# Optimization experiments

Hardware: AMD Instinct MI355X
Metric: run time of the kernel (lower is better)

The kernel has to match this reference:

```python
import jax, jax.numpy as jnp
import numpy as np

HIDDEN = 450
DEPTH = 6
ATOM_FDIM = 35          # len(ELEM_LIST)+6+5+1
BOND_FDIM = 5
MAX_NB = 15
N_ATOMS = 20000
N_BONDS = 40000
N_MESS = 16000          # tree messages (row 0 is the zero padding slot)
N_MOLS = 1000


def _linear_init(key, out_dim, in_dim):
    s = 1.0 / np.sqrt(in_dim)
    return jax.random.uniform(key, (out_dim, in_dim), jnp.float32, -s, s)


def setup_inputs() -> dict:
    key = jax.random.key(0)
    ks = jax.random.split(key, 9)
    total_msg = N_MESS + N_BONDS
    fatoms = jax.random.normal(ks[0], (N_ATOMS, ATOM_FDIM), jnp.float32)
    fbonds = jax.random.normal(ks[1], (N_BONDS, ATOM_FDIM + BOND_FDIM), jnp.float32)
    agraph = jax.random.randint(ks[2], (N_ATOMS, MAX_NB), 0, total_msg, jnp.int32)
    bgraph = jax.random.randint(ks[3], (N_BONDS, MAX_NB), 0, total_msg, jnp.int32)
    tree_message = jax.random.normal(ks[4], (N_MESS, HIDDEN), jnp.float32)
    tree_message = tree_message.at[0].set(0.0)  # index 0 = padding message
    # uniform scope: N_MOLS molecules of N_ATOMS//N_MOLS atoms each
    mol_ids = jnp.repeat(jnp.arange(N_MOLS, dtype=jnp.int32), N_ATOMS // N_MOLS)
    W_i = _linear_init(ks[5], HIDDEN, ATOM_FDIM + BOND_FDIM)
    W_h = _linear_init(ks[6], HIDDEN, HIDDEN)
    W_o = _linear_init(ks[7], HIDDEN, ATOM_FDIM + HIDDEN)
    s = 1.0 / np.sqrt(ATOM_FDIM + HIDDEN)
    b_o = jax.random.uniform(ks[8], (HIDDEN,), jnp.float32, -s, s)
    return {"fatoms": fatoms, "fbonds": fbonds, "agraph": agraph, "bgraph": bgraph,
            "mol_ids": mol_ids, "n_mols": N_MOLS, "tree_message": tree_message,
            "W_i": W_i, "W_h": W_h, "W_o": W_o, "b_o": b_o}


def reference(fatoms, fbonds, agraph, bgraph, mol_ids, n_mols, tree_message,
              W_i, W_h, W_o, b_o):
    binput = fbonds @ W_i.T                       # [B, H]
    graph_message = jax.nn.relu(binput)
    for _ in range(DEPTH - 1):                    # static depth loop
        message = jnp.concatenate([tree_message, graph_message], axis=0)  # [M+B, H]
        nei_message = message[bgraph].sum(axis=1)  # gather [B, MAX_NB, H] -> [B, H]
        graph_message = jax.nn.relu(binput + nei_message @ W_h.T)
    message = jnp.concatenate([tree_message, graph_message], axis=0)
    nei_message = message[agraph].sum(axis=1)      # [A, H]
    ainput = jnp.concatenate([fatoms, nei_message], axis=1)  # [A, ATOM_FDIM+H]
    atom_hiddens = jax.nn.relu(ainput @ W_o.T + b_o)          # [A, H]
    # mean over each molecule's atoms (scope)
    sums = jax.ops.segment_sum(atom_hiddens, mol_ids, num_segments=n_mols)
    counts = jax.ops.segment_sum(jnp.ones((atom_hiddens.shape[0], 1), atom_hiddens.dtype),
                                 mol_ids, num_segments=n_mols)
    return sums / counts
```

## Files before the change

### kernel.cpp

```cpp
#include <hip/hip_runtime.h>

#define HIDDEN 450
#define MAX_NB 15
#define N_ATOMS 20000
#define N_BONDS 40000
#define N_MESS  16000
#define N_MOLS  1000
#define KPAD    512
#define MSTRIDE 456

typedef unsigned int uint;
typedef unsigned short ushort;
typedef __bf16 bf16x8 __attribute__((ext_vector_type(8)));
typedef float  f32x4  __attribute__((ext_vector_type(4)));

__device__ __forceinline__ ushort f2bf(float f) {
    uint u = __builtin_bit_cast(uint, f);
    u += 0x7fffu + ((u >> 16) & 1u);
    return (ushort)(u >> 16);
}
__device__ __forceinline__ float bfhi(uint w) {
    return __builtin_bit_cast(float, w & 0xffff0000u);
}
__device__ __forceinline__ float bflo(uint w) {
    return __builtin_bit_cast(float, w << 16);
}


__global__ __launch_bounds__(256) void pack_tree(const float* __restrict__ tree,
                                                 ushort* __restrict__ tbuf) {
    const int r = blockIdx.x, t = threadIdx.x;
    if (t < 228) {
        uint p = 0;
        if (t < 225) {
            const float2 v = *(const float2*)&tree[(size_t)r * HIDDEN + 2 * t];
            p = (uint)f2bf(v.x) | ((uint)f2bf(v.y) << 16);
        }
        ((uint*)(tbuf + (size_t)r * MSTRIDE))[t] = p;
    }
}

__global__ __launch_bounds__(256) void pack_bonds(const float* __restrict__ fbonds,
                                                  ushort* __restrict__ Abuf) {
    const int r = blockIdx.x * 4 + (threadIdx.x >> 6);
    const int t = threadIdx.x & 63;
    if (r >= N_BONDS) return;
    ushort* row = Abuf + (size_t)r * KPAD;
    if (t < 40) row[t] = f2bf(fbonds[(size_t)r * 40 + t]);
    else        row[t] = 0;
    if (t < 16) row[496 + t] = 0;
}

__global__ __launch_bounds__(256) void pack_atoms(const float* __restrict__ fatoms,
                                                  ushort* __restrict__ Aout) {
    const int r = blockIdx.x * 4 + (threadIdx.x >> 6);
    const int t = threadIdx.x & 63;
    if (r >= N_ATOMS) return;
    ushort* row = Aout + (size_t)r * KPAD;
    if (t < 40) row[t] = (t < 35) ? f2bf(fatoms[(size_t)r * 35 + t]) : (ushort)0;
    if (t < 16) row[496 + t] = 0;
}

__global__ __launch_bounds__(256) void pack_w(const float* __restrict__ W_i,
                                              const float* __restrict__ W_h,
                                              const float* __restrict__ W_o,
                                              ushort* __restrict__ Wcat,
                                              ushort* __restrict__ Wocat) {
    const int n = blockIdx.x;
    for (int c = threadIdx.x; c < KPAD; c += 256) {
        float v = 0.0f, vo = 0.0f;
        if (n < HIDDEN) {
            if (c < 40)       v = W_i[(size_t)n * 40 + c];
            else if (c < 490) v = W_h[(size_t)n * HIDDEN + (c - 40)];
            if (c < 35)       vo = W_o[(size_t)n * 485 + c];
            else if (c >= 40 && c < 490) vo = W_o[(size_t)n * 485 + 35 + (c - 40)];
        }
        Wcat [(size_t)n * KPAD + c] = f2bf(v);
        Wocat[(size_t)n * KPAD + c] = f2bf(vo);
    }
}

__global__ __launch_bounds__(256) void precompute_base(const int* __restrict__ g,
                                                       const ushort* __restrict__ tbuf,
                                                       ushort* __restrict__ base,
                                                       int nrows) {
    const int r = blockIdx.x * 4 + (threadIdx.x >> 6);
    const int lane = threadIdx.x & 63;
    if (r >= nrows) return;
    const int* gr = g + (size_t)r * MAX_NB;
    int idx[MAX_NB];
#pragma unroll
    for (int j = 0; j < MAX_NB; ++j) idx[j] = gr[j];
    if (lane >= 57) return;
    const int off = lane * 8;
    float acc[8] = {};
#pragma unroll
    for (int j = 0; j < MAX_NB; ++j) {
        if (idx[j] < N_MESS) {
            const uint4 w = *(const uint4*)(tbuf + (size_t)idx[j] * MSTRIDE + off);
            acc[0] += bflo(w.x); acc[1] += bfhi(w.x);
            acc[2] += bflo(w.y); acc[3] += bfhi(w.y);
            acc[4] += bflo(w.z); acc[5] += bfhi(w.z);
            acc[6] += bflo(w.w); acc[7] += bfhi(w.w);
        }
    }
    uint4 p;
    p.x = (uint)f2bf(acc[0]) | ((uint)f2bf(acc[1]) << 16);
    p.y = (uint)f2bf(acc[2]) | ((uint)f2bf(acc[3]) << 16);
    p.z = (uint)f2bf(acc[4]) | ((uint)f2bf(acc[5]) << 16);
    p.w = (uint)f2bf(acc[6]) | ((uint)f2bf(acc[7]) << 16);
    *(uint4*)(base + (size_t)r * MSTRIDE + off) = p;
}

__global__ __launch_bounds__(256) void gather_dyn(const int* __restrict__ g,
                                                  const ushort* __restrict__ base,
                                                  const ushort* __restrict__ gmsg,
                                                  ushort* __restrict__ dst, int nrows) {
    const int r = blockIdx.x * 4 + (threadIdx.x >> 6);
    const int lane = threadIdx.x & 63;
    if (r >= nrows) return;
    const int* gr = g + (size_t)r * MAX_NB;
    int idx[MAX_NB];
#pragma unroll
    for (int j = 0; j < MAX_NB; ++j) idx[j] = gr[j];
    if (lane >= 57) return;
    const int off = lane * 8;
    const uint4 b = *(const uint4*)(base + (size_t)r * MSTRIDE + off);
    float acc[8];
    acc[0] = bflo(b.x); acc[1] = bfhi(b.x);
    acc[2] = bflo(b.y); acc[3] = bfhi(b.y);
    acc[4] = bflo(b.z); acc[5] = bfhi(b.z);
    acc[6] = bflo(b.w); acc[7] = bfhi(b.w);
#pragma unroll
    for (int j = 0; j < MAX_NB; ++j) {
        if (idx[j] >= N_MESS) {
            const uint4 w = *(const uint4*)(gmsg + (size_t)(idx[j] - N_MESS) * MSTRIDE + off);
            acc[0] += bflo(w.x); acc[1] += bfhi(w.x);
            acc[2] += bflo(w.y); acc[3] += bfhi(w.y);
            acc[4] += bflo(w.z); acc[5] += bfhi(w.z);
            acc[6] += bflo(w.w); acc[7] += bfhi(w.w);
        }
    }
    uint4 p;
    p.x = (uint)f2bf(acc[0]) | ((uint)f2bf(acc[1]) << 16);
    p.y = (uint)f2bf(acc[2]) | ((uint)f2bf(acc[3]) << 16);
    p.z = (uint)f2bf(acc[4]) | ((uint)f2bf(acc[5]) << 16);
    p.w = (uint)f2bf(acc[6]) | ((uint)f2bf(acc[7]) << 16);
    *(uint4*)(dst + (size_t)r * KPAD + 40 + off) = p;
}

template <int MODE, int KT>
__global__ __launch_bounds__(256, 2) void mfma_gemm(
    const ushort* __restrict__ A, int M,
    const ushort* __restrict__ W,
    const float* __restrict__ bias, const int* __restrict__ mol_ids,
    ushort* __restrict__ gout, float* __restrict__ aout, int mtiles) {
    __shared__ ushort At[64 * KT * 32];
    const int tid = threadIdx.x;
    const int id  = blockIdx.x;
    const int b     = id & 7;
    const int n_blk = (id >> 3) & 1;
    const int m_blk = (id >> 4) * 8 + b;
    if (m_blk >= mtiles) return;
    const int m0 = m_blk * 64, n0 = n_blk * 256;
    const int CPR = KT * 4;

    {
        const int srow = tid >> 2;
        const int c0   = tid & 3;
        const ushort* gsrc = A + (size_t)min(m0 + srow, M - 1) * KPAD;
        ushort* lrow = At + srow * (KT * 32);
#pragma unroll
        for (int c = c0; c < CPR; c += 4) {
            const uint4 v = *(const uint4*)(gsrc + c * 8);
            *(uint4*)&lrow[(c ^ (srow & 7)) * 8] = v;
        }
    }
    __syncthreads();

    const int lane = tid & 63;
    const int wave = tid >> 6;
    const int wn = wave * 64;
    const int lr = lane & 15;
    const int lk = lane >> 4;

    size_t woff[4];
#pragma unroll
    for (int s = 0; s < 4; ++s)
        woff[s] = (size_t)(n0 + wn + s * 16 + lr) * KPAD + lk * 8;

    f32x4 acc[4][4];
#pragma unroll
    for (int i = 0; i < 4; ++i)
#pragma unroll
        for (int j = 0; j < 4; ++j) acc[i][j] = (f32x4){0.f, 0.f, 0.f, 0.f};

    bf16x8 wa[4], wb[4], afa[4];
#pragma unroll
    for (int s = 0; s < 4; ++s) wa[s] = *(const bf16x8*)&W[woff[s]];
#pragma unroll
    for (int s = 0; s < 4; ++s)
        wb[s] = (KT > 1) ? *(const bf16x8*)&W[woff[s] + 32] : wa[s];
#pragma unroll
    for (int mt = 0; mt < 4; ++mt) {
        const int row = mt * 16 + lr;
        afa[mt] = *(const bf16x8*)&At[(row * CPR + (lk ^ (row & 7))) * 8];
    }

#pragma unroll
    for (int i = 0; i < KT; ++i) {
        bf16x8 wc[4], afb[4];
        if (i + 2 < KT) {
#pragma unroll
            for (int s = 0; s < 4; ++s)
                wc[s] = *(const bf16x8*)&W[woff[s] + (size_t)(i + 2) * 32];
        }
        if (i + 1 < KT) {
#pragma unroll
            for (int mt = 0; mt < 4; ++mt) {
                const int row = mt * 16 + lr;
                const int chunk = (((i + 1) * 4 + lk)) ^ (row & 7);
                afb[mt] = *(const bf16x8*)&At[(row * CPR + chunk) * 8];
            }
        }
#pragma unroll
        for (int mt = 0; mt < 4; ++mt)
#pragma unroll
            for (int nt = 0; nt < 4; ++nt)
                acc[mt][nt] = __builtin_amdgcn_mfma_f32_16x16x32_bf16(
                    afa[mt], wa[nt], acc[mt][nt], 0, 0, 0);
        if (i + 1 < KT) {
#pragma unroll
            for (int s = 0; s < 4; ++s) wa[s] = wb[s];
#pragma unroll
            for (int mt = 0; mt < 4; ++mt) afa[mt] = afb[mt];
        }
        if (i + 2 < KT) {
#pragma unroll
            for (int s = 0; s < 4; ++s) wb[s] = wc[s];
        }
    }

    const int col_l = lane & 15;
    const int rbase = (lane >> 4) * 4;
#pragma unroll
    for (int mt = 0; mt < 4; ++mt) {
        const int mbase = m0 + mt * 16 + rbase;
        int mol[4];
        if (MODE == 1) {
#pragma unroll
            for (int reg = 0; reg < 4; ++reg)
                mol[reg] = mol_ids[min(mbase + reg, M - 1)];
        }
#pragma unroll
        for (int nt = 0; nt < 4; ++nt) {
            const int n = n0 + wn + nt * 16 + col_l;
            if (MODE == 0) {
#pragma unroll
                for (int reg = 0; reg < 4; ++reg) {
                    const int m = mbase + reg;
                    if (m >= M) continue;
                    if (n < HIDDEN)
                        gout[(size_t)m * MSTRIDE + n] = f2bf(fmaxf(acc[mt][nt][reg], 0.0f));
                    else if (n < MSTRIDE)
                        gout[(size_t)m * MSTRIDE + n] = 0;
                }
            } else {
                if (n >= HIDDEN) continue;
                const float bsum = bias[n];
                float run = 0.0f;
                int cur = mol[0];
#pragma unroll
                for (int reg = 0; reg < 4; ++reg) {
                    const float v = (mbase + reg < M)
                        ? fmaxf(acc[mt][nt][reg] + bsum, 0.0f) : 0.0f;
                    if (mol[reg] != cur) {
                        atomicAdd(&aout[(size_t)cur * HIDDEN + n], run);
                        cur = mol[reg];
                        run = 0.0f;
                    }
                    run += v;
                }
                atomicAdd(&aout[(size_t)cur * HIDDEN + n], run);
            }
        }
    }
}

__global__ __launch_bounds__(256) void count_atoms(const int* __restrict__ mol_ids,
                                                   float* __restrict__ counts) {
    const int a = blockIdx.x * 256 + threadIdx.x;
    if (a < N_ATOMS) atomicAdd(&counts[mol_ids[a]], 1.0f);
}
__global__ __launch_bounds__(256) void div_counts(float* __restrict__ out,
                                                  const float* __restrict__ counts) {
    const int i = blockIdx.x * 256 + threadIdx.x;
    if (i < N_MOLS * HIDDEN) out[i] = out[i] / counts[i / HIDDEN];
}

extern "C" void kernel_launch(void* const* d_in, const int* in_sizes, int n_in,
                              void* d_out, int out_size, void* d_ws, size_t ws_size,
                              hipStream_t stream) {
    const float* fatoms  = (const float*)d_in[0];
    const float* fbonds  = (const float*)d_in[1];
    const int*   agraph  = (const int*)d_in[2];
    const int*   bgraph  = (const int*)d_in[3];
    const int*   mol_ids = (const int*)d_in[4];
    const float* tree    = (const float*)d_in[6];
    const float* W_i     = (const float*)d_in[7];
    const float* W_h     = (const float*)d_in[8];
    const float* W_o     = (const float*)d_in[9];
    const float* b_o     = (const float*)d_in[10];
    float* out = (float*)d_out;

    ushort* Abuf   = (ushort*)d_ws;
    ushort* Aout   = Abuf   + (size_t)N_BONDS * KPAD;
    ushort* gmsg   = Aout   + (size_t)N_ATOMS * KPAD;
    ushort* tbuf   = gmsg   + (size_t)N_BONDS * MSTRIDE;
    ushort* Wcat   = tbuf   + (size_t)N_MESS  * MSTRIDE;
    ushort* Wocat  = Wcat   + (size_t)KPAD * KPAD;
    ushort* base_b = Wocat  + (size_t)KPAD * KPAD;
    ushort* base_a = base_b + (size_t)N_BONDS * MSTRIDE;
    float*  counts = (float*)(base_a + (size_t)N_ATOMS * MSTRIDE);

    (void)hipMemsetAsync(d_out, 0, (size_t)N_MOLS * HIDDEN * sizeof(float), stream);
    (void)hipMemsetAsync(counts, 0, N_MOLS * sizeof(float), stream);

    const dim3 blk(256);
    pack_tree <<<N_MESS, blk, 0, stream>>>(tree, tbuf);
    pack_bonds<<<(N_BONDS + 3) / 4, blk, 0, stream>>>(fbonds, Abuf);
    pack_atoms<<<(N_ATOMS + 3) / 4, blk, 0, stream>>>(fatoms, Aout);
    pack_w    <<<KPAD, blk, 0, stream>>>(W_i, W_h, W_o, Wcat, Wocat);
    precompute_base<<<(N_BONDS + 3) / 4, blk, 0, stream>>>(bgraph, tbuf, base_b, N_BONDS);
    precompute_base<<<(N_ATOMS + 3) / 4, blk, 0, stream>>>(agraph, tbuf, base_a, N_ATOMS);

    const int mtB = (N_BONDS + 63) / 64;
    const int mtA = (N_ATOMS + 63) / 64;
    const dim3 gB(((mtB + 7) / 8) * 16);
    const dim3 gA(((mtA + 7) / 8) * 16);

    mfma_gemm<0, 2><<<gB, blk, 0, stream>>>(Abuf, N_BONDS, Wcat,
                                            nullptr, nullptr, gmsg, nullptr, mtB);
    for (int it = 0; it < 5; ++it) {
        gather_dyn<<<(N_BONDS + 3) / 4, blk, 0, stream>>>(bgraph, base_b, gmsg,
                                                          Abuf, N_BONDS);
        mfma_gemm<0, 16><<<gB, blk, 0, stream>>>(Abuf, N_BONDS, Wcat,
                                                 nullptr, nullptr, gmsg, nullptr, mtB);
    }
    gather_dyn<<<(N_ATOMS + 3) / 4, blk, 0, stream>>>(agraph, base_a, gmsg,
                                                      Aout, N_ATOMS);
    mfma_gemm<1, 16><<<gA, blk, 0, stream>>>(Aout, N_ATOMS, Wocat,
                                             b_o, mol_ids, nullptr, out, mtA);

    count_atoms<<<(N_ATOMS + 255) / 256, blk, 0, stream>>>(mol_ids, counts);
    div_counts <<<(N_MOLS * HIDDEN + 255) / 256, blk, 0, stream>>>(out, counts);
}
```

Baseline: 921.4 us.

## Fuse neighbor gather into MFMA GEMM with ping-pong message buffers

Fuses each message-passing gather into the following GEMM. Each 512-thread block gathers its 64 rows directly into shared memory, then all 8 waves cover the full N range, replacing the earlier two-block N split. This removes the global round-trip of the gathered A matrix (write then re-read 40000x512 bf16 per iteration) and the launches that went with it. Ping-pong gmsg buffers avoid read/write races between rows of the same pass. The costs are that each block now gathers serially before any MFMA work, occupancy drops with 512-thread blocks, and the grid has fewer blocks.

Result: slower. 1.017 ms (+10.4%).

```diff
diff --git a/kernel.cpp b/kernel.cpp
--- a/kernel.cpp
+++ b/kernel.cpp
@@ -40,25 +40,12 @@
     }
 }
 
-__global__ __launch_bounds__(256) void pack_bonds(const float* __restrict__ fbonds,
-                                                  ushort* __restrict__ Abuf) {
+__global__ __launch_bounds__(256) void pack_feats(const float* __restrict__ src, int fd,
+                                                  ushort* __restrict__ dst, int nrows) {
     const int r = blockIdx.x * 4 + (threadIdx.x >> 6);
     const int t = threadIdx.x & 63;
-    if (r >= N_BONDS) return;
-    ushort* row = Abuf + (size_t)r * KPAD;
-    if (t < 40) row[t] = f2bf(fbonds[(size_t)r * 40 + t]);
-    else        row[t] = 0;
-    if (t < 16) row[496 + t] = 0;
-}
-
-__global__ __launch_bounds__(256) void pack_atoms(const float* __restrict__ fatoms,
-                                                  ushort* __restrict__ Aout) {
-    const int r = blockIdx.x * 4 + (threadIdx.x >> 6);
-    const int t = threadIdx.x & 63;
-    if (r >= N_ATOMS) return;
-    ushort* row = Aout + (size_t)r * KPAD;
-    if (t < 40) row[t] = (t < 35) ? f2bf(fatoms[(size_t)r * 35 + t]) : (ushort)0;
-    if (t < 16) row[496 + t] = 0;
+    if (r >= nrows) return;
+    dst[(size_t)r * 64 + t] = (t < fd) ? f2bf(src[(size_t)r * fd + t]) : (ushort)0;
 }
 
 __global__ __launch_bounds__(256) void pack_w(const float* __restrict__ W_i,
@@ -112,82 +99,83 @@
     *(uint4*)(base + (size_t)r * MSTRIDE + off) = p;
 }
 
-__global__ __launch_bounds__(256) void gather_dyn(const int* __restrict__ g,
-                                                  const ushort* __restrict__ base,
-                                                  const ushort* __restrict__ gmsg,
-                                                  ushort* __restrict__ dst, int nrows) {
-    const int r = blockIdx.x * 4 + (threadIdx.x >> 6);
-    const int lane = threadIdx.x & 63;
-    if (r >= nrows) return;
-    const int* gr = g + (size_t)r * MAX_NB;
-    int idx[MAX_NB];
-#pragma unroll
-    for (int j = 0; j < MAX_NB; ++j) idx[j] = gr[j];
-    if (lane >= 57) return;
-    const int off = lane * 8;
-    const uint4 b = *(const uint4*)(base + (size_t)r * MSTRIDE + off);
-    float acc[8];
-    acc[0] = bflo(b.x); acc[1] = bfhi(b.x);
-    acc[2] = bflo(b.y); acc[3] = bfhi(b.y);
-    acc[4] = bflo(b.z); acc[5] = bfhi(b.z);
-    acc[6] = bflo(b.w); acc[7] = bfhi(b.w);
-#pragma unroll
-    for (int j = 0; j < MAX_NB; ++j) {
-        if (idx[j] >= N_MESS) {
-            const uint4 w = *(const uint4*)(gmsg + (size_t)(idx[j] - N_MESS) * MSTRIDE + off);
-            acc[0] += bflo(w.x); acc[1] += bfhi(w.x);
-            acc[2] += bflo(w.y); acc[3] += bfhi(w.y);
-            acc[4] += bflo(w.z); acc[5] += bfhi(w.z);
-            acc[6] += bflo(w.w); acc[7] += bfhi(w.w);
-        }
-    }
-    uint4 p;
-    p.x = (uint)f2bf(acc[0]) | ((uint)f2bf(acc[1]) << 16);
-    p.y = (uint)f2bf(acc[2]) | ((uint)f2bf(acc[3]) << 16);
-    p.z = (uint)f2bf(acc[4]) | ((uint)f2bf(acc[5]) << 16);
-    p.w = (uint)f2bf(acc[6]) | ((uint)f2bf(acc[7]) << 16);
-    *(uint4*)(dst + (size_t)r * KPAD + 40 + off) = p;
-}
-
-template <int MODE, int KT>
-__global__ __launch_bounds__(256, 2) void mfma_gemm(
-    const ushort* __restrict__ A, int M,
-    const ushort* __restrict__ W,
-    const float* __restrict__ bias, const int* __restrict__ mol_ids,
-    ushort* __restrict__ gout, float* __restrict__ aout, int mtiles) {
+template <int MODE, int GATHER, int KT>
+__global__ __launch_bounds__(512, 2) void fused_mp(
+    const int* __restrict__ g, const ushort* __restrict__ base,
+    const ushort* __restrict__ feats, const ushort* __restrict__ gin,
+    const ushort* __restrict__ W, const float* __restrict__ bias,
+    const int* __restrict__ mol_ids, ushort* __restrict__ gout,
+    float* __restrict__ aout, int M, int mtiles) {
     __shared__ ushort At[64 * KT * 32];
-    const int tid = threadIdx.x;
-    const int id  = blockIdx.x;
-    const int b     = id & 7;
-    const int n_blk = (id >> 3) & 1;
-    const int m_blk = (id >> 4) * 8 + b;
+    const int m_blk = blockIdx.x;
     if (m_blk >= mtiles) return;
-    const int m0 = m_blk * 64, n0 = n_blk * 256;
-    const int CPR = KT * 4;
-
-    {
-        const int srow = tid >> 2;
-        const int c0   = tid & 3;
-        const ushort* gsrc = A + (size_t)min(m0 + srow, M - 1) * KPAD;
-        ushort* lrow = At + srow * (KT * 32);
-#pragma unroll
-        for (int c = c0; c < CPR; c += 4) {
-            const uint4 v = *(const uint4*)(gsrc + c * 8);
-            *(uint4*)&lrow[(c ^ (srow & 7)) * 8] = v;
-        }
-    }
-    __syncthreads();
-
+    const int m0 = m_blk * 64;
+    const int tid  = threadIdx.x;
     const int lane = tid & 63;
     const int wave = tid >> 6;
+
+    if (GATHER) {
+#pragma unroll 1
+        for (int rr = 0; rr < 8; ++rr) {
+            const int row = rr * 8 + wave;
+            const int r = min(m0 + row, M - 1);
+            const int* gr = g + (size_t)r * MAX_NB;
+            int idx[MAX_NB];
+#pragma unroll
+            for (int j = 0; j < MAX_NB; ++j) idx[j] = gr[j];
+            ushort* lrow = At + row * (KT * 32);
+            const int sw = row & 7;
+            if (lane < 57) {
+                const int off = lane * 8;
+                const uint4 b4 = *(const uint4*)(base + (size_t)r * MSTRIDE + off);
+                float acc[8];
+                acc[0] = bflo(b4.x); acc[1] = bfhi(b4.x);
+                acc[2] = bflo(b4.y); acc[3] = bfhi(b4.y);
+                acc[4] = bflo(b4.z); acc[5] = bfhi(b4.z);
+                acc[6] = bflo(b4.w); acc[7] = bfhi(b4.w);
+#pragma unroll
+                for (int j = 0; j < MAX_NB; ++j) {
+                    if (idx[j] >= N_MESS) {
+                        const uint4 w4 = *(const uint4*)(gin +
+                            (size_t)(idx[j] - N_MESS) * MSTRIDE + off);
+                        acc[0] += bflo(w4.x); acc[1] += bfhi(w4.x);
+                        acc[2] += bflo(w4.y); acc[3] += bfhi(w4.y);
+                        acc[4] += bflo(w4.z); acc[5] += bfhi(w4.z);
+                        acc[6] += bflo(w4.w); acc[7] += bfhi(w4.w);
+                    }
+                }
+                uint4 p;
+                p.x = (uint)f2bf(acc[0]) | ((uint)f2bf(acc[1]) << 16);
+                p.y = (uint)f2bf(acc[2]) | ((uint)f2bf(acc[3]) << 16);
+                p.z = (uint)f2bf(acc[4]) | ((uint)f2bf(acc[5]) << 16);
+                p.w = (uint)f2bf(acc[6]) | ((uint)f2bf(acc[7]) << 16);
+                *(uint4*)&lrow[((5 + lane) ^ sw) * 8] = p;
+            } else if (lane < 62) {
+                const int c = lane - 57;
+                const uint4 f = *(const uint4*)(feats + (size_t)r * 64 + c * 8);
+                *(uint4*)&lrow[(c ^ sw) * 8] = f;
+            } else {
+                const uint4 z = {0, 0, 0, 0};
+                *(uint4*)&lrow[(lane ^ sw) * 8] = z;
+            }
+        }
+    } else {
+        const int row = tid >> 3, c = tid & 7;
+        const int r = min(m0 + row, M - 1);
+        const uint4 f = *(const uint4*)(feats + (size_t)r * 64 + c * 8);
+        *(uint4*)&At[row * (KT * 32) + ((c ^ (row & 7)) * 8)] = f;
+    }
+    __syncthreads();
+
     const int wn = wave * 64;
     const int lr = lane & 15;
     const int lk = lane >> 4;
+    const int CPR = KT * 4;
 
     size_t woff[4];
 #pragma unroll
     for (int s = 0; s < 4; ++s)
-        woff[s] = (size_t)(n0 + wn + s * 16 + lr) * KPAD + lk * 8;
+        woff[s] = (size_t)(wn + s * 16 + lr) * KPAD + lk * 8;
 
     f32x4 acc[4][4];
 #pragma unroll
@@ -204,7 +192,7 @@
 #pragma unroll
     for (int mt = 0; mt < 4; ++mt) {
         const int row = mt * 16 + lr;
-        afa[mt] = *(const bf16x8*)&At[(row * CPR + (lk ^ (row & 7))) * 8];
+        afa[mt] = *(const bf16x8*)&At[row * (KT * 32) + ((lk ^ (row & 7)) * 8)];
     }
 
 #pragma unroll
@@ -219,8 +207,8 @@
 #pragma unroll
             for (int mt = 0; mt < 4; ++mt) {
                 const int row = mt * 16 + lr;
-                const int chunk = (((i + 1) * 4 + lk)) ^ (row & 7);
-                afb[mt] = *(const bf16x8*)&At[(row * CPR + chunk) * 8];
+                const int chunk = ((i + 1) * 4 + lk) ^ (row & 7);
+                afb[mt] = *(const bf16x8*)&At[row * (KT * 32) + chunk * 8];
             }
         }
 #pragma unroll
@@ -254,7 +242,7 @@
         }
 #pragma unroll
         for (int nt = 0; nt < 4; ++nt) {
-            const int n = n0 + wn + nt * 16 + col_l;
+            const int n = wn + nt * 16 + col_l;
             if (MODE == 0) {
 #pragma unroll
                 for (int reg = 0; reg < 4; ++reg) {
@@ -313,10 +301,11 @@
     const float* b_o     = (const float*)d_in[10];
     float* out = (float*)d_out;
 
-    ushort* Abuf   = (ushort*)d_ws;
-    ushort* Aout   = Abuf   + (size_t)N_BONDS * KPAD;
-    ushort* gmsg   = Aout   + (size_t)N_ATOMS * KPAD;
-    ushort* tbuf   = gmsg   + (size_t)N_BONDS * MSTRIDE;
+    ushort* featsB = (ushort*)d_ws;
+    ushort* featsA = featsB + (size_t)N_BONDS * 64;
+    ushort* gmsgA  = featsA + (size_t)N_ATOMS * 64;
+    ushort* gmsgB  = gmsgA  + (size_t)N_BONDS * MSTRIDE;
+    ushort* tbuf   = gmsgB  + (size_t)N_BONDS * MSTRIDE;
     ushort* Wcat   = tbuf   + (size_t)N_MESS  * MSTRIDE;
     ushort* Wocat  = Wcat   + (size_t)KPAD * KPAD;
     ushort* base_b = Wocat  + (size_t)KPAD * KPAD;
@@ -328,29 +317,28 @@
 
     const dim3 blk(256);
     pack_tree <<<N_MESS, blk, 0, stream>>>(tree, tbuf);
-    pack_bonds<<<(N_BONDS + 3) / 4, blk, 0, stream>>>(fbonds, Abuf);
-    pack_atoms<<<(N_ATOMS + 3) / 4, blk, 0, stream>>>(fatoms, Aout);
+    pack_feats<<<(N_BONDS + 3) / 4, blk, 0, stream>>>(fbonds, 40, featsB, N_BONDS);
+    pack_feats<<<(N_ATOMS + 3) / 4, blk, 0, stream>>>(fatoms, 35, featsA, N_ATOMS);
     pack_w    <<<KPAD, blk, 0, stream>>>(W_i, W_h, W_o, Wcat, Wocat);
     precompute_base<<<(N_BONDS + 3) / 4, blk, 0, stream>>>(bgraph, tbuf, base_b, N_BONDS);
     precompute_base<<<(N_ATOMS + 3) / 4, blk, 0, stream>>>(agraph, tbuf, base_a, N_ATOMS);
 
     const int mtB = (N_BONDS + 63) / 64;
     const int mtA = (N_ATOMS + 63) / 64;
-    const dim3 gB(((mtB + 7) / 8) * 16);
-    const dim3 gA(((mtA + 7) / 8) * 16);
-
-    mfma_gemm<0, 2><<<gB, blk, 0, stream>>>(Abuf, N_BONDS, Wcat,
-                                            nullptr, nullptr, gmsg, nullptr, mtB);
+    const dim3 blk512(512);
+
+    fused_mp<0, 0, 2><<<mtB, blk512, 0, stream>>>(
+        nullptr, nullptr, featsB, nullptr, Wcat,
+        nullptr, nullptr, gmsgA, nullptr, N_BONDS, mtB);
+    ushort* pp[6] = {gmsgA, gmsgB, gmsgA, gmsgB, gmsgA, gmsgB};
     for (int it = 0; it < 5; ++it) {
-        gather_dyn<<<(N_BONDS + 3) / 4, blk, 0, stream>>>(bgraph, base_b, gmsg,
-                                                          Abuf, N_BONDS);
-        mfma_gemm<0, 16><<<gB, blk, 0, stream>>>(Abuf, N_BONDS, Wcat,
-                                                 nullptr, nullptr, gmsg, nullptr, mtB);
-    }
-    gather_dyn<<<(N_ATOMS + 3) / 4, blk, 0, stream>>>(agraph, base_a, gmsg,
-                                                      Aout, N_ATOMS);
-    mfma_gemm<1, 16><<<gA, blk, 0, stream>>>(Aout, N_ATOMS, Wocat,
-                                             b_o, mol_ids, nullptr, out, mtA);
+        fused_mp<0, 1, 16><<<mtB, blk512, 0, stream>>>(
+            bgraph, base_b, featsB, pp[it], Wcat,
+            nullptr, nullptr, pp[it + 1], nullptr, N_BONDS, mtB);
+    }
+    fused_mp<1, 1, 16><<<mtA, blk512, 0, stream>>>(
+        agraph, base_a, featsA, pp[5], Wocat,
+        b_o, mol_ids, nullptr, out, N_ATOMS, mtA);
 
     count_atoms<<<(N_ATOMS + 255) / 256, blk, 0, stream>>>(mol_ids, counts);
     div_counts <<<(N_MOLS * HIDDEN + 255) / 256, blk, 0, stream>>>(out, counts);
```

## Enlarge GEMM blocks to 128-row tiles with 512 threads and deeper prefetch

Applied to the files above, without the earlier changes.

The MFMA GEMM now runs 512-thread blocks covering 128 rows instead of 64, so each block shares its weight-column work across twice as many rows. Only the first 64 rows are staged in shared memory. Waves handling the second 64 rows load their A fragments straight from global memory. The weight prefetch pipeline is deepened by one stage, and the A prefetch now also runs two steps ahead. The grouped block-index swizzle is dropped in favour of a plain linear mapping, which gives up L2 locality tuning and makes half the waves depend on uncached-by-LDS global reads.

After: 1.133 ms. 23.0% more time.

```diff
diff --git a/kernel.cpp b/kernel.cpp
--- a/kernel.cpp
+++ b/kernel.cpp
@@ -150,7 +150,7 @@
 }
 
 template <int MODE, int KT>
-__global__ __launch_bounds__(256, 2) void mfma_gemm(
+__global__ __launch_bounds__(512) void mfma_gemm(
     const ushort* __restrict__ A, int M,
     const ushort* __restrict__ W,
     const float* __restrict__ bias, const int* __restrict__ mol_ids,
@@ -158,36 +158,41 @@
     __shared__ ushort At[64 * KT * 32];
     const int tid = threadIdx.x;
     const int id  = blockIdx.x;
-    const int b     = id & 7;
-    const int n_blk = (id >> 3) & 1;
-    const int m_blk = (id >> 4) * 8 + b;
+    const int n_blk = id & 1;
+    const int m_blk = id >> 1;
     if (m_blk >= mtiles) return;
-    const int m0 = m_blk * 64, n0 = n_blk * 256;
+    const int m0 = m_blk * 128, n0 = n_blk * 256;
     const int CPR = KT * 4;
 
     {
-        const int srow = tid >> 2;
-        const int c0   = tid & 3;
+        const int srow = tid >> 3;
+        const int c0   = tid & 7;
         const ushort* gsrc = A + (size_t)min(m0 + srow, M - 1) * KPAD;
         ushort* lrow = At + srow * (KT * 32);
-#pragma unroll
-        for (int c = c0; c < CPR; c += 4) {
-            const uint4 v = *(const uint4*)(gsrc + c * 8);
-            *(uint4*)&lrow[(c ^ (srow & 7)) * 8] = v;
-        }
+        uint4 tmp[KT / 2 > 0 ? (KT + 1) / 2 : 1];
+#pragma unroll
+        for (int i = 0; i < KT / 2; ++i)
+            tmp[i] = *(const uint4*)(gsrc + (c0 + 8 * i) * 8);
+#pragma unroll
+        for (int i = 0; i < KT / 2; ++i)
+            *(uint4*)&lrow[((c0 + 8 * i) ^ (srow & 7)) * 8] = tmp[i];
     }
     __syncthreads();
 
     const int lane = tid & 63;
     const int wave = tid >> 6;
-    const int wn = wave * 64;
+    const int mh = wave >> 2;
+    const int nq = wave & 3;
+    const int wn = n0 + nq * 64;
     const int lr = lane & 15;
     const int lk = lane >> 4;
 
-    size_t woff[4];
-#pragma unroll
-    for (int s = 0; s < 4; ++s)
-        woff[s] = (size_t)(n0 + wn + s * 16 + lr) * KPAD + lk * 8;
+    size_t woff[4], ahoff[4];
+#pragma unroll
+    for (int s = 0; s < 4; ++s) {
+        woff[s]  = (size_t)(wn + s * 16 + lr) * KPAD + lk * 8;
+        ahoff[s] = (size_t)min(m0 + 64 + s * 16 + lr, M - 1) * KPAD + lk * 8;
+    }
 
     f32x4 acc[4][4];
 #pragma unroll
@@ -195,34 +200,42 @@
 #pragma unroll
         for (int j = 0; j < 4; ++j) acc[i][j] = (f32x4){0.f, 0.f, 0.f, 0.f};
 
-    bf16x8 wa[4], wb[4], afa[4];
+    auto loadA = [&](int i, bf16x8* dst) {
+        if (mh == 0) {
+#pragma unroll
+            for (int mt = 0; mt < 4; ++mt) {
+                const int row = mt * 16 + lr;
+                const int chunk = (i * 4 + lk) ^ (row & 7);
+                dst[mt] = *(const bf16x8*)&At[row * (KT * 32) + chunk * 8];
+            }
+        } else {
+#pragma unroll
+            for (int mt = 0; mt < 4; ++mt)
+                dst[mt] = *(const bf16x8*)&A[ahoff[mt] + (size_t)i * 32];
+        }
+    };
+
+    bf16x8 wa[4], wb[4], wc[4], afa[4], afb[4];
 #pragma unroll
     for (int s = 0; s < 4; ++s) wa[s] = *(const bf16x8*)&W[woff[s]];
 #pragma unroll
     for (int s = 0; s < 4; ++s)
         wb[s] = (KT > 1) ? *(const bf16x8*)&W[woff[s] + 32] : wa[s];
 #pragma unroll
-    for (int mt = 0; mt < 4; ++mt) {
-        const int row = mt * 16 + lr;
-        afa[mt] = *(const bf16x8*)&At[(row * CPR + (lk ^ (row & 7))) * 8];
-    }
+    for (int s = 0; s < 4; ++s)
+        wc[s] = (KT > 2) ? *(const bf16x8*)&W[woff[s] + 64] : wa[s];
+    loadA(0, afa);
+    if (KT > 1) loadA(1, afb);
 
 #pragma unroll
     for (int i = 0; i < KT; ++i) {
-        bf16x8 wc[4], afb[4];
-        if (i + 2 < KT) {
+        bf16x8 wd[4], afc[4];
+        if (i + 3 < KT) {
 #pragma unroll
             for (int s = 0; s < 4; ++s)
-                wc[s] = *(const bf16x8*)&W[woff[s] + (size_t)(i + 2) * 32];
-        }
-        if (i + 1 < KT) {
-#pragma unroll
-            for (int mt = 0; mt < 4; ++mt) {
-                const int row = mt * 16 + lr;
-                const int chunk = (((i + 1) * 4 + lk)) ^ (row & 7);
-                afb[mt] = *(const bf16x8*)&At[(row * CPR + chunk) * 8];
-            }
-        }
+                wd[s] = *(const bf16x8*)&W[woff[s] + (size_t)(i + 3) * 32];
+        }
+        if (i + 2 < KT) loadA(i + 2, afc);
 #pragma unroll
         for (int mt = 0; mt < 4; ++mt)
 #pragma unroll
@@ -231,13 +244,17 @@
                     afa[mt], wa[nt], acc[mt][nt], 0, 0, 0);
         if (i + 1 < KT) {
 #pragma unroll
-            for (int s = 0; s < 4; ++s) wa[s] = wb[s];
+            for (int s = 0; s < 4; ++s) { wa[s] = wb[s]; wb[s] = wc[s]; }
 #pragma unroll
             for (int mt = 0; mt < 4; ++mt) afa[mt] = afb[mt];
         }
+        if (i + 3 < KT) {
+#pragma unroll
+            for (int s = 0; s < 4; ++s) wc[s] = wd[s];
+        }
         if (i + 2 < KT) {
 #pragma unroll
-            for (int s = 0; s < 4; ++s) wb[s] = wc[s];
+            for (int mt = 0; mt < 4; ++mt) afb[mt] = afc[mt];
         }
     }
 
@@ -245,7 +262,7 @@
     const int rbase = (lane >> 4) * 4;
 #pragma unroll
     for (int mt = 0; mt < 4; ++mt) {
-        const int mbase = m0 + mt * 16 + rbase;
+        const int mbase = m0 + mh * 64 + mt * 16 + rbase;
         int mol[4];
         if (MODE == 1) {
 #pragma unroll
@@ -254,7 +271,7 @@
         }
 #pragma unroll
         for (int nt = 0; nt < 4; ++nt) {
-            const int n = n0 + wn + nt * 16 + col_l;
+            const int n = wn + nt * 16 + col_l;
             if (MODE == 0) {
 #pragma unroll
                 for (int reg = 0; reg < 4; ++reg) {
@@ -334,23 +351,24 @@
     precompute_base<<<(N_BONDS + 3) / 4, blk, 0, stream>>>(bgraph, tbuf, base_b, N_BONDS);
     precompute_base<<<(N_ATOMS + 3) / 4, blk, 0, stream>>>(agraph, tbuf, base_a, N_ATOMS);
 
-    const int mtB = (N_BONDS + 63) / 64;
-    const int mtA = (N_ATOMS + 63) / 64;
-    const dim3 gB(((mtB + 7) / 8) * 16);
-    const dim3 gA(((mtA + 7) / 8) * 16);
-
-    mfma_gemm<0, 2><<<gB, blk, 0, stream>>>(Abuf, N_BONDS, Wcat,
-                                            nullptr, nullptr, gmsg, nullptr, mtB);
+    const int mtB = (N_BONDS + 127) / 128;
+    const int mtA = (N_ATOMS + 127) / 128;
+    const dim3 gB(mtB * 2);
+    const dim3 gA(mtA * 2);
+    const dim3 blk512(512);
+
+    mfma_gemm<0, 2><<<gB, blk512, 0, stream>>>(Abuf, N_BONDS, Wcat,
+                                               nullptr, nullptr, gmsg, nullptr, mtB);
     for (int it = 0; it < 5; ++it) {
         gather_dyn<<<(N_BONDS + 3) / 4, blk, 0, stream>>>(bgraph, base_b, gmsg,
                                                           Abuf, N_BONDS);
-        mfma_gemm<0, 16><<<gB, blk, 0, stream>>>(Abuf, N_BONDS, Wcat,
-                                                 nullptr, nullptr, gmsg, nullptr, mtB);
+        mfma_gemm<0, 16><<<gB, blk512, 0, stream>>>(Abuf, N_BONDS, Wcat,
+                                                    nullptr, nullptr, gmsg, nullptr, mtB);
     }
     gather_dyn<<<(N_ATOMS + 3) / 4, blk, 0, stream>>>(agraph, base_a, gmsg,
                                                       Aout, N_ATOMS);
-    mfma_gemm<1, 16><<<gA, blk, 0, stream>>>(Aout, N_ATOMS, Wocat,
-                                             b_o, mol_ids, nullptr, out, mtA);
+    mfma_gemm<1, 16><<<gA, blk512, 0, stream>>>(Aout, N_ATOMS, Wocat,
+                                                b_o, mol_ids, nullptr, out, mtA);
 
     count_atoms<<<(N_ATOMS + 255) / 256, blk, 0, stream>>>(mol_ids, counts);
     div_counts <<<(N_MOLS * HIDDEN + 255) / 256, blk, 0, stream>>>(out, counts);
```
